# Optimization experiments

Hardware: AMD Instinct MI355X
Metric: run time of the kernel (lower is better)

Reference implementation:

```python
import jax, jax.numpy as jnp
import numpy as np

B, K, C, Q, NCLS = 16, 36, 2048, 1024, 16
LIN = 1024
DIN = 2 * C + 16 + Q  # 5136


def _linear_params(key, din, dout, scale=0.02):
    kw, kb = jax.random.split(key)
    W = jax.random.normal(kw, (din, dout), dtype=jnp.float32) * scale
    b = jax.random.normal(kb, (dout,), dtype=jnp.float32) * scale
    return W, b


def setup_inputs() -> dict:
    key = jax.random.key(0)
    ks = jax.random.split(key, 12)
    box_feats = jax.random.normal(ks[0], (B, K, C), dtype=jnp.float32)
    q_feats = jax.random.normal(ks[1], (B, Q), dtype=jnp.float32)
    # valid boxes: x2>x1, y2>y1 so areas are strictly positive (no div-by-zero)
    x1y1 = jax.random.uniform(ks[2], (B, K, 2), dtype=jnp.float32)
    wh = jax.random.uniform(ks[3], (B, K, 2), dtype=jnp.float32, minval=0.05, maxval=1.0)
    box_coords = jnp.concatenate([x1y1, x1y1 + wh, wh], axis=-1)  # [B,K,6]
    index = jax.random.randint(ks[4], (B,), 1, K + 1)  # ragged box counts in [1,K]
    wholefeat = jax.random.normal(ks[5], (B, C), dtype=jnp.float32)
    pooled = jax.random.normal(ks[6], (B, C), dtype=jnp.float32)
    W1, b1 = _linear_params(ks[7], DIN, LIN)
    W2, b2 = _linear_params(ks[8], LIN, LIN)
    W3, b3 = _linear_params(ks[9], LIN, LIN)
    Wf1, bf1 = _linear_params(ks[10], LIN, LIN // 2)
    Wf2, bf2 = _linear_params(ks[11], LIN // 2, NCLS)
    return {"wholefeat": wholefeat, "pooled": pooled, "box_feats": box_feats,
            "q_feats": q_feats, "box_coords": box_coords, "index": index,
            "W1": W1, "b1": b1, "W2": W2, "b2": b2, "W3": W3, "b3": b3,
            "Wf1": Wf1, "bf1": bf1, "Wf2": Wf2, "bf2": bf2}


def _rn_forward(box_feats, q_feats, box_coords, index,
                W1, b1, W2, b2, W3, b3, Wf1, bf1, Wf2, bf2):
    b_, k_, c_ = box_feats.shape
    # ragged -> padded + mask: pair (i,j) valid iff i < index[b] and j < index[b]
    valid = (jnp.arange(k_)[None, :] < index[:, None]).astype(box_feats.dtype)  # [B,K]
    pair_mask = valid[:, :, None] * valid[:, None, :]  # [B,K,K]

    # pairwise dot of region features
    dot = jnp.einsum('bid,bjd->bij', box_feats, box_feats)[..., None]  # [B,K,K,1]

    bc = box_coords  # [B,K,6]
    area = (bc[..., 2] - bc[..., 0]) * (bc[..., 3] - bc[..., 1])  # [B,K]
    lr = jnp.maximum(0.0, jnp.minimum(bc[:, :, None, 2], bc[:, None, :, 2])
                     - jnp.maximum(bc[:, :, None, 0], bc[:, None, :, 0]))
    ud = jnp.maximum(0.0, jnp.minimum(bc[:, :, None, 3], bc[:, None, :, 3])
                     - jnp.maximum(bc[:, :, None, 1], bc[:, None, :, 1]))
    overlap = lr * ud  # [B,K,K]
    area_i = area[:, :, None]
    area_j = area[:, None, :]
    iou = (overlap / (area_i + area_j - overlap))[..., None]
    o_ij = (overlap / area_i)[..., None]
    o_ji = (overlap / area_j)[..., None]

    b_ij = jnp.broadcast_to(bc[:, :, None, :], (b_, k_, k_, 6))
    b_ji = jnp.broadcast_to(bc[:, None, :, :], (b_, k_, k_, 6))
    o_i = jnp.broadcast_to(box_feats[:, :, None, :], (b_, k_, k_, c_))
    o_j = jnp.broadcast_to(box_feats[:, None, :, :], (b_, k_, k_, c_))
    qst = jnp.broadcast_to(q_feats[:, None, None, :], (b_, k_, k_, q_feats.shape[-1]))

    # [B,K,K,5136] = [o_i, o_j, qst, dot, b_ij, b_ji, iou, o_ij, o_ji]
    feat = jnp.concatenate([o_i, o_j, qst, dot, b_ij, b_ji, iou, o_ij, o_ji], axis=-1)

    h = jax.nn.relu(feat @ W1 + b1)
    h = jax.nn.relu(h @ W2 + b2)
    h = jax.nn.relu(h @ W3 + b3)  # [B,K,K,1024]

    # masked sum-pool over all valid (i,j) pairs
    g = jnp.einsum('bijh,bij->bh', h, pair_mask)  # [B,1024]

    out = jax.nn.relu(g @ Wf1 + bf1) @ Wf2 + bf2  # [B,Ncls]
    return out


def reference(wholefeat, pooled, box_feats, q_feats, box_coords, index,
              W1, b1, W2, b2, W3, b3, Wf1, bf1, Wf2, bf2):
    # wholefeat / pooled are unused by the original forward as well
    return _rn_forward(box_feats, q_feats, box_coords, index,
                       W1, b1, W2, b2, W3, b3, Wf1, bf1, Wf2, bf2)
```

## Files before the change

kernel.cpp:

```cpp
#include <hip/hip_runtime.h>
#include <stdint.h>

typedef unsigned short u16;
typedef __attribute__((ext_vector_type(8))) short short8;
typedef __attribute__((ext_vector_type(4))) float f32x4;

#define Bn 16
#define Kn 36
#define Cn 2048
#define Qn 1024
#define LINn 1024
#define NPp 1296
#define NPAIRn 20736
#define NBIn 576

__device__ __forceinline__ u16 f2bf(float f) {
  union { float f; unsigned int u; } v; v.f = f;
  unsigned int r = v.u + 0x7FFFu + ((v.u >> 16) & 1u);
  return (u16)(r >> 16);
}

__device__ __forceinline__ void llds16(const void* g, void* l) {
  __builtin_amdgcn_global_load_lds((const __attribute__((address_space(1))) void*)g,
                                   (__attribute__((address_space(3))) void*)l, 16, 0, 0);
}

__global__ void k_transpose_all(const float* __restrict__ W1, const float* __restrict__ W2,
                                const float* __restrict__ W3, u16* __restrict__ W1abT,
                                u16* __restrict__ W2T, u16* __restrict__ W3T) {
  __shared__ float tile[32][33];
  int z = blockIdx.z;
  const float* src; u16* dst; int ld_dst;
  if (z == 0)      { if (blockIdx.y >= 32) return; src = W2; dst = W2T; ld_dst = 1024; }
  else if (z == 1) { if (blockIdx.y >= 32) return; src = W3; dst = W3T; ld_dst = 1024; }
  else if (z == 2) { src = W1; dst = W1abT; ld_dst = 2048; }
  else             { src = W1 + (size_t)2048 * 1024; dst = W1abT + (size_t)1024 * 2048; ld_dst = 2048; }
  int n0 = blockIdx.x * 32, k0 = blockIdx.y * 32;
  int tx = threadIdx.x & 31, ty = threadIdx.x >> 5;
#pragma unroll
  for (int r = 0; r < 32; r += 8)
    tile[ty + r][tx] = src[(size_t)(k0 + ty + r) * 1024 + (n0 + tx)];
  __syncthreads();
#pragma unroll
  for (int r = 0; r < 32; r += 8)
    dst[(size_t)(n0 + ty + r) * ld_dst + (k0 + tx)] = f2bf(tile[tx][ty + r]);
}

__global__ void k_f2b(const float4* __restrict__ src, ushort4* __restrict__ dst, int n4) {
  int i = blockIdx.x * 256 + threadIdx.x;
  if (i < n4) {
    float4 v = src[i];
    ushort4 o;
    o.x = f2bf(v.x); o.y = f2bf(v.y); o.z = f2bf(v.z); o.w = f2bf(v.w);
    dst[i] = o;
  }
}

__global__ void k_build(const int* __restrict__ index, int* __restrict__ pairList,
                        int* __restrict__ batchC, int* __restrict__ cnt2) {
  __shared__ int offs[17];
  int tid = threadIdx.x;
  if (tid == 0) {
    int o = 0;
    for (int b = 0; b < Bn; ++b) { offs[b] = o; int v = index[b]; o += v * v; }
    offs[16] = o;
    cnt2[0] = o;
    cnt2[1] = (o + 127) & ~127;
  }
  __syncthreads();
  int total = offs[16];
  int totalPad = (total + 127) & ~127;
  for (int b = 0; b < Bn; ++b) {
    int v = index[b]; int n = v * v; int base = offs[b];
    for (int t = tid; t < n; t += 256) {
      int i = t / v, j = t - i * v;
      pairList[base + t] = b * NPp + i * Kn + j;
      batchC[base + t] = b;
    }
  }
  for (int t = total + tid; t < totalPad; t += 256) {
    pairList[t] = 0;
    batchC[t] = 0;
  }
}

__global__ void k_pcinit(const float* __restrict__ b1, float* __restrict__ Pc) {
  int n = blockIdx.x * 256 + threadIdx.x;
  float v = b1[n];
#pragma unroll
  for (int b = 0; b < Bn; ++b) Pc[b * LINn + n] = v;
}

__global__ void k_pconst(const float* __restrict__ q, const float* __restrict__ W1,
                         float* __restrict__ Pc) {
  __shared__ float qs[Bn][32];
  int n = blockIdx.x * 256 + threadIdx.x;
  int k0 = blockIdx.y * 32;
  const float* Wq = W1 + (size_t)(2 * Cn) * LINn;
  for (int t = threadIdx.x; t < Bn * 32; t += 256) {
    int b = t >> 5, k = t & 31;
    qs[b][k] = q[b * Qn + k0 + k];
  }
  __syncthreads();
  float acc[Bn];
#pragma unroll
  for (int b = 0; b < Bn; ++b) acc[b] = 0.f;
  for (int k = 0; k < 32; ++k) {
    float w = Wq[(size_t)(k0 + k) * LINn + n];
#pragma unroll
    for (int b = 0; b < Bn; ++b) acc[b] += qs[b][k] * w;
  }
#pragma unroll
  for (int b = 0; b < Bn; ++b) atomicAdd(&Pc[b * LINn + n], acc[b]);
}

__global__ void k_pairscalars(const float* __restrict__ bfm, const float* __restrict__ bc,
                              const int* __restrict__ pairList, const int* __restrict__ cnt2,
                              float* __restrict__ dotC, float* __restrict__ iouC,
                              float* __restrict__ oijC, float* __restrict__ ojiC) {
  int cnt = cnt2[0];
  int lane = threadIdx.x & 63;
  for (int m = blockIdx.x * 4 + (threadIdx.x >> 6); m < cnt; m += gridDim.x * 4) {
    int p = pairList[m];
    int b = p / NPp, rem = p - b * NPp, i = rem / Kn, j = rem - (rem / Kn) * Kn;
    const float4* Ai = (const float4*)(bfm + (size_t)(b * Kn + i) * Cn);
    const float4* Aj = (const float4*)(bfm + (size_t)(b * Kn + j) * Cn);
    float s = 0.f;
#pragma unroll
    for (int t = 0; t < Cn / 4 / 64; ++t) {
      float4 x = Ai[lane + t * 64], y = Aj[lane + t * 64];
      s += x.x * y.x + x.y * y.y + x.z * y.z + x.w * y.w;
    }
#pragma unroll
    for (int o = 32; o > 0; o >>= 1) s += __shfl_down(s, o);
    if (lane == 0) {
      const float* ci = bc + (size_t)(b * Kn + i) * 6;
      const float* cj = bc + (size_t)(b * Kn + j) * 6;
      float ai = (ci[2] - ci[0]) * (ci[3] - ci[1]);
      float aj = (cj[2] - cj[0]) * (cj[3] - cj[1]);
      float lr = fmaxf(0.f, fminf(ci[2], cj[2]) - fmaxf(ci[0], cj[0]));
      float ud = fmaxf(0.f, fminf(ci[3], cj[3]) - fmaxf(ci[1], cj[1]));
      float ov = lr * ud;
      dotC[m] = s;
      iouC[m] = ov / (ai + aj - ov);
      oijC[m] = ov / ai;
      ojiC[m] = ov / aj;
    }
  }
}

__global__ void k_padd(const float* __restrict__ P12s, const float* __restrict__ Pc,
                       const float* __restrict__ bc, const float* __restrict__ W1,
                       float* __restrict__ P12) {
  int bi = blockIdx.x;
  int b = bi / Kn;
  const float* c = bc + (size_t)bi * 6;
  const float* W = W1 + (size_t)(2 * Cn + Qn + 1) * LINn;
  const size_t SL = (size_t)640 * 2048;
#pragma unroll
  for (int it = 0; it < 8; ++it) {
    int cc = it * 256 + threadIdx.x;
    size_t idx = (size_t)bi * 2048 + cc;
    float s = P12s[idx] + P12s[SL + idx] + P12s[2 * SL + idx] + P12s[3 * SL + idx];
    int n = cc & 1023;
    int rbase = (cc < 1024) ? 0 : 6;
    float a = 0.f;
#pragma unroll
    for (int t = 0; t < 6; ++t) a += c[t] * W[(size_t)(rbase + t) * LINn + n];
    if (cc < 1024) a += Pc[b * LINn + n];
    P12[idx] = s + a;
  }
}

__global__ void k_h1(const float* __restrict__ P12,
                     const float* __restrict__ dotC, const float* __restrict__ iouC,
                     const float* __restrict__ oijC, const float* __restrict__ ojiC,
                     const int* __restrict__ pairList, const int* __restrict__ cnt2,
                     const float* __restrict__ W1, u16* __restrict__ H1) {
  int cnt = cnt2[0];
  int t = threadIdx.x;
  const float4* wd = (const float4*)(W1 + (size_t)(2 * Cn + Qn) * LINn);
  const float4* wu = (const float4*)(W1 + (size_t)(2 * Cn + Qn + 13) * LINn);
  const float4* wa = (const float4*)(W1 + (size_t)(2 * Cn + Qn + 14) * LINn);
  const float4* wb = (const float4*)(W1 + (size_t)(2 * Cn + Qn + 15) * LINn);
  float4 e1 = wd[t], e2 = wu[t], e3 = wa[t], e4 = wb[t];
  for (int m = blockIdx.x; m < cnt; m += gridDim.x) {
    int p = pairList[m];
    int b = p / NPp, rem = p - b * NPp, i = rem / Kn, j = rem - (rem / Kn) * Kn;
    float d = dotC[m], u = iouC[m], o1 = oijC[m], o2 = ojiC[m];
    const float4* p1 = (const float4*)(P12 + (size_t)(b * Kn + i) * 2048);
    const float4* p2 = (const float4*)(P12 + (size_t)(b * Kn + j) * 2048 + 1024);
    ushort4* outp = (ushort4*)(H1 + (size_t)m * 1024);
    float4 v1 = p1[t], v2 = p2[t];
    ushort4 o;
    o.x = f2bf(fmaxf(v1.x + v2.x + d * e1.x + u * e2.x + o1 * e3.x + o2 * e4.x, 0.f));
    o.y = f2bf(fmaxf(v1.y + v2.y + d * e1.y + u * e2.y + o1 * e3.y + o2 * e4.y, 0.f));
    o.z = f2bf(fmaxf(v1.z + v2.z + d * e1.z + u * e2.z + o1 * e3.z + o2 * e4.z, 0.f));
    o.w = f2bf(fmaxf(v1.w + v2.w + d * e1.w + u * e2.w + o1 * e3.w + o2 * e4.w, 0.f));
    outp[t] = o;
  }
}

template <int EPI>
__global__ void __launch_bounds__(256) k_gemm(
    const u16* __restrict__ A, const u16* __restrict__ BT,
    int N, int K, int KC, int Mvalid, const int* __restrict__ cnt2,
    float* __restrict__ Cf, int CfSlice, u16* __restrict__ Cb,
    const float* __restrict__ bias,
    const int* __restrict__ batchC, float* __restrict__ G) {
  __shared__ u16 Alds[2][128 * 64];
  __shared__ u16 Blds[2][64 * 64];
  __shared__ float Gpart[(EPI == 2) ? (Bn * 64) : 4];

  const int tid = threadIdx.x;
  const int wave = tid >> 6, lane = tid & 63;
  const int m0 = blockIdx.x * 128;
  const int n0 = blockIdx.y * 64;
  const int wm = (wave >> 1) * 64, wn = (wave & 1) * 32;

  int Mv = Mvalid;
  if (EPI != 0) {
    Mv = cnt2[0];
    if (m0 >= Mv) return;
  }
  if (EPI == 2) {
    for (int t = tid; t < Bn * 64; t += 256) Gpart[t] = 0.f;
  }

  f32x4 zero = {0.f, 0.f, 0.f, 0.f};
  f32x4 acc[4][2];
#pragma unroll
  for (int x = 0; x < 4; ++x)
#pragma unroll
    for (int y = 0; y < 2; ++y) acc[x][y] = zero;

  const int srow = tid >> 3;
  const int sslot = ((tid & 7) ^ (srow & 7)) * 16;
  const size_t ldb = (size_t)K * 2;

  auto stage = [&](int buf, int k0) {
    char* aB = (char*)Alds[buf] + wave * 1024;
    char* bB = (char*)Blds[buf] + wave * 1024;
#pragma unroll
    for (int c = 0; c < 4; ++c) {
      int rg = m0 + c * 32 + srow; if (rg >= Mv) rg = Mv - 1;
      llds16((const char*)A + (size_t)rg * ldb + (size_t)k0 * 2 + sslot, aB + c * 4096);
    }
#pragma unroll
    for (int c = 0; c < 2; ++c) {
      int rg = n0 + c * 32 + srow;
      llds16((const char*)BT + (size_t)rg * ldb + (size_t)k0 * 2 + sslot, bB + c * 4096);
    }
  };

  const int kbeg = blockIdx.z * KC;
  const int kend = kbeg + KC;
  stage(0, kbeg);
  asm volatile("s_waitcnt vmcnt(0)");
  __syncthreads();
  int cur = 0;
  for (int k0 = kbeg; k0 < kend; k0 += 64) {
    if (k0 + 64 < kend) stage(cur ^ 1, k0 + 64);
    const char* Ab = (const char*)Alds[cur];
    const char* Bb = (const char*)Blds[cur];
    short8 af[2][4], bfr[2][2];
#pragma unroll
    for (int kk = 0; kk < 2; ++kk) {
#pragma unroll
      for (int f = 0; f < 4; ++f) {
        int rA = wm + f * 16 + (lane & 15);
        int sl = ((kk * 4 + (lane >> 4)) ^ (rA & 7)) * 16;
        af[kk][f] = *(const short8*)(Ab + (size_t)rA * 128 + sl);
      }
#pragma unroll
      for (int f = 0; f < 2; ++f) {
        int rB = wn + f * 16 + (lane & 15);
        int sl = ((kk * 4 + (lane >> 4)) ^ (rB & 7)) * 16;
        bfr[kk][f] = *(const short8*)(Bb + (size_t)rB * 128 + sl);
      }
    }
#pragma unroll
    for (int kk = 0; kk < 2; ++kk)
#pragma unroll
      for (int x = 0; x < 4; ++x)
#pragma unroll
        for (int y = 0; y < 2; ++y)
          acc[x][y] = __builtin_amdgcn_mfma_f32_16x16x32_bf16(af[kk][x], bfr[kk][y],
                                                              acc[x][y], 0, 0, 0);
    asm volatile("s_waitcnt vmcnt(0)");
    __syncthreads();
    cur ^= 1;
  }

  if (EPI == 0) {
    float* Cs = Cf + (size_t)blockIdx.z * CfSlice;
#pragma unroll
    for (int x = 0; x < 4; ++x) {
      int rb = m0 + wm + x * 16 + (lane >> 4) * 4;
#pragma unroll
      for (int r = 0; r < 4; ++r) {
        int row = rb + r;
        if (row < Mv) {
#pragma unroll
          for (int y = 0; y < 2; ++y)
            Cs[(size_t)row * N + (n0 + wn + y * 16 + (lane & 15))] = acc[x][y][r];
        }
      }
    }
  } else if (EPI == 1) {
#pragma unroll
    for (int x = 0; x < 4; ++x) {
      int rb = m0 + wm + x * 16 + (lane >> 4) * 4;
#pragma unroll
      for (int r = 0; r < 4; ++r) {
        int row = rb + r;
#pragma unroll
        for (int y = 0; y < 2; ++y) {
          int col = n0 + wn + y * 16 + (lane & 15);
          Cb[(size_t)row * N + col] = f2bf(fmaxf(acc[x][y][r] + bias[col], 0.f));
        }
      }
    }
  } else {
    const int cnt = Mv;
#pragma unroll
    for (int x = 0; x < 4; ++x) {
      int rb = m0 + wm + x * 16 + (lane >> 4) * 4;
      int b0 = batchC[rb], b1 = batchC[rb + 1], b2 = batchC[rb + 2], b3 = batchC[rb + 3];
      float mk0 = (rb     < cnt) ? 1.f : 0.f;
      float mk1 = (rb + 1 < cnt) ? 1.f : 0.f;
      float mk2 = (rb + 2 < cnt) ? 1.f : 0.f;
      float mk3 = (rb + 3 < cnt) ? 1.f : 0.f;
#pragma unroll
      for (int y = 0; y < 2; ++y) {
        int coll = wn + y * 16 + (lane & 15);
        float bs = bias[n0 + coll];
        float s0 = mk0 * fmaxf(acc[x][y][0] + bs, 0.f);
        float s1 = mk1 * fmaxf(acc[x][y][1] + bs, 0.f);
        float s2 = mk2 * fmaxf(acc[x][y][2] + bs, 0.f);
        float s3 = mk3 * fmaxf(acc[x][y][3] + bs, 0.f);
        if (b0 == b3) {
          atomicAdd(&Gpart[b0 * 64 + coll], s0 + s1 + s2 + s3);
        } else {
          atomicAdd(&Gpart[b0 * 64 + coll], s0);
          atomicAdd(&Gpart[b1 * 64 + coll], s1);
          atomicAdd(&Gpart[b2 * 64 + coll], s2);
          atomicAdd(&Gpart[b3 * 64 + coll], s3);
        }
      }
    }
    __syncthreads();
    for (int t = tid; t < Bn * 64; t += 256) {
      float v = Gpart[t];
      if (v != 0.f) atomicAdd(&G[(t >> 6) * LINn + n0 + (t & 63)], v);
    }
  }
}

__global__ void k_final1(const float* __restrict__ G, const float* __restrict__ Wf1,
                         float* __restrict__ S) {
  __shared__ float g[128];
  int b = blockIdx.x, kz = blockIdx.y, tid = threadIdx.x;
  if (tid < 128) g[tid] = G[b * 1024 + kz * 128 + tid];
  __syncthreads();
  float acc = 0.f;
  const float* W = Wf1 + (size_t)(kz * 128) * 512 + tid;
  for (int k = 0; k < 128; ++k) acc += g[k] * W[(size_t)k * 512];
  atomicAdd(&S[b * 512 + tid], acc);
}

__global__ void k_final2(const float* __restrict__ S, const float* __restrict__ bf1,
                         const float* __restrict__ Wf2, const float* __restrict__ bf2,
                         float* __restrict__ out) {
  __shared__ float mid[512];
  __shared__ float part[256];
  int b = blockIdx.x, tid = threadIdx.x;
  for (int t = tid; t < 512; t += 256) mid[t] = fmaxf(S[b * 512 + t] + bf1[t], 0.f);
  __syncthreads();
  int o = tid & 15, seg = tid >> 4;
  float s = 0.f;
#pragma unroll
  for (int t = 0; t < 32; ++t) {
    int j = seg * 32 + t;
    s += mid[j] * Wf2[j * 16 + o];
  }
  part[tid] = s;
  __syncthreads();
  if (tid < 16) {
    float v = bf2[tid];
#pragma unroll
    for (int sg = 0; sg < 16; ++sg) v += part[sg * 16 + tid];
    out[b * 16 + tid] = v;
  }
}

extern "C" void kernel_launch(void* const* d_in, const int* in_sizes, int n_in,
                              void* d_out, int out_size, void* d_ws, size_t ws_size,
                              hipStream_t stream) {
  const float* box_feats  = (const float*)d_in[2];
  const float* q_feats    = (const float*)d_in[3];
  const float* box_coords = (const float*)d_in[4];
  const int*   index      = (const int*)d_in[5];
  const float* W1  = (const float*)d_in[6];
  const float* b1  = (const float*)d_in[7];
  const float* W2  = (const float*)d_in[8];
  const float* b2  = (const float*)d_in[9];
  const float* W3  = (const float*)d_in[10];
  const float* b3  = (const float*)d_in[11];
  const float* Wf1 = (const float*)d_in[12];
  const float* bf1 = (const float*)d_in[13];
  const float* Wf2 = (const float*)d_in[14];
  const float* bf2 = (const float*)d_in[15];
  float* out = (float*)d_out;

  char* ws = (char*)d_ws;
  size_t off = 0;
  auto alloc = [&](size_t bytes) { void* p = ws + off; off += (bytes + 255) & ~(size_t)255; return p; };
  u16* W1abT = (u16*)alloc((size_t)2048 * 2048 * 2);
  u16* W2T   = (u16*)alloc((size_t)1024 * 1024 * 2);
  u16* W3T   = (u16*)alloc((size_t)1024 * 1024 * 2);
  u16* BFb   = (u16*)alloc((size_t)NBIn * Cn * 2);
  float* P12s = (float*)alloc((size_t)4 * 640 * 2048 * 4);
  float* P12  = (float*)alloc((size_t)NBIn * 2048 * 4);
  float* Pc   = (float*)alloc((size_t)Bn * LINn * 4);
  float* dotC = (float*)alloc((size_t)NPAIRn * 4);
  float* iouC = (float*)alloc((size_t)NPAIRn * 4);
  float* oijC = (float*)alloc((size_t)NPAIRn * 4);
  float* ojiC = (float*)alloc((size_t)NPAIRn * 4);
  int* pairList = (int*)alloc((size_t)NPAIRn * 4);
  int* batchC   = (int*)alloc((size_t)NPAIRn * 4);
  int* cnt2     = (int*)alloc(64);
  float* G  = (float*)alloc((size_t)Bn * LINn * 4);
  float* S  = (float*)alloc((size_t)Bn * 512 * 4);
  u16* H1 = (u16*)alloc((size_t)NPAIRn * 1024 * 2);
  u16* H2 = (u16*)alloc((size_t)NPAIRn * 1024 * 2);

  k_transpose_all<<<dim3(32, 64, 4), 256, 0, stream>>>(W1, W2, W3, W1abT, W2T, W3T);
  k_f2b<<<(NBIn * Cn / 4 + 255) / 256, 256, 0, stream>>>((const float4*)box_feats,
                                                         (ushort4*)BFb, NBIn * Cn / 4);
  k_build<<<1, 256, 0, stream>>>(index, pairList, batchC, cnt2);
  k_pcinit<<<4, 256, 0, stream>>>(b1, Pc);
  k_pconst<<<dim3(4, 32), 256, 0, stream>>>(q_feats, W1, Pc);
  k_pairscalars<<<648, 256, 0, stream>>>(box_feats, box_coords, pairList, cnt2,
                                         dotC, iouC, oijC, ojiC);
  k_gemm<0><<<dim3(5, 32, 4), 256, 0, stream>>>(BFb, W1abT, 2048, 2048, 512, NBIn, nullptr,
                                                P12s, 640 * 2048, nullptr, nullptr,
                                                nullptr, nullptr);
  k_padd<<<NBIn, 256, 0, stream>>>(P12s, Pc, box_coords, W1, P12);
  k_h1<<<2592, 256, 0, stream>>>(P12, dotC, iouC, oijC, ojiC, pairList, cnt2, W1, H1);
  hipMemsetAsync(G, 0, (size_t)Bn * LINn * 4, stream);
  hipMemsetAsync(S, 0, (size_t)Bn * 512 * 4, stream);
  k_gemm<1><<<dim3(162, 16, 1), 256, 0, stream>>>(H1, W2T, 1024, 1024, 1024, 0, cnt2,
                                                  nullptr, 0, H2, b2, nullptr, nullptr);
  k_gemm<2><<<dim3(162, 16, 1), 256, 0, stream>>>(H2, W3T, 1024, 1024, 1024, 0, cnt2,
                                                  nullptr, 0, nullptr, b3, batchC, G);
  k_final1<<<dim3(16, 8), 512, 0, stream>>>(G, Wf1, S);
  k_final2<<<16, 256, 0, stream>>>(S, bf1, Wf2, bf2, out);
}
```

Measured before the change: 161.6 us.

## Triple-buffer GEMM LDS pipeline and remap blocks by XCD for active tiles

```diff
diff --git a/kernel.cpp b/kernel.cpp
--- a/kernel.cpp
+++ b/kernel.cpp
@@ -208,20 +208,30 @@
     float* __restrict__ Cf, int CfSlice, u16* __restrict__ Cb,
     const float* __restrict__ bias,
     const int* __restrict__ batchC, float* __restrict__ G) {
-  __shared__ u16 Alds[2][128 * 64];
-  __shared__ u16 Blds[2][64 * 64];
+  __shared__ u16 Alds[3][128 * 64];
+  __shared__ u16 Blds[3][64 * 64];
   __shared__ float Gpart[(EPI == 2) ? (Bn * 64) : 4];
 
   const int tid = threadIdx.x;
   const int wave = tid >> 6, lane = tid & 63;
-  const int m0 = blockIdx.x * 128;
-  const int n0 = blockIdx.y * 64;
   const int wm = (wave >> 1) * 64, wn = (wave & 1) * 32;
 
   int Mv = Mvalid;
-  if (EPI != 0) {
+  int m0, n0;
+  if (EPI == 0) {
+    m0 = blockIdx.x * 128;
+    n0 = blockIdx.y * 64;
+  } else {
     Mv = cnt2[0];
-    if (m0 >= Mv) return;
+    int nMt = (Mv + 127) >> 7;
+    int nact = nMt * 16;
+    int id = blockIdx.x;
+    if (id >= nact) return;
+    int q = nact >> 3, r = nact & 7;
+    int xcd = id & 7, rank = id >> 3;
+    int wg = (xcd < r ? xcd * (q + 1) : r * (q + 1) + (xcd - r) * q) + rank;
+    m0 = (wg >> 4) * 128;
+    n0 = (wg & 15) * 64;
   }
   if (EPI == 2) {
     for (int t = tid; t < Bn * 64; t += 256) Gpart[t] = 0.f;
@@ -253,16 +263,9 @@
     }
   };
 
-  const int kbeg = blockIdx.z * KC;
-  const int kend = kbeg + KC;
-  stage(0, kbeg);
-  asm volatile("s_waitcnt vmcnt(0)");
-  __syncthreads();
-  int cur = 0;
-  for (int k0 = kbeg; k0 < kend; k0 += 64) {
-    if (k0 + 64 < kend) stage(cur ^ 1, k0 + 64);
-    const char* Ab = (const char*)Alds[cur];
-    const char* Bb = (const char*)Blds[cur];
+  auto compute = [&](int buf) {
+    const char* Ab = (const char*)Alds[buf];
+    const char* Bb = (const char*)Blds[buf];
     short8 af[2][4], bfr[2][2];
 #pragma unroll
     for (int kk = 0; kk < 2; ++kk) {
@@ -287,10 +290,26 @@
         for (int y = 0; y < 2; ++y)
           acc[x][y] = __builtin_amdgcn_mfma_f32_16x16x32_bf16(af[kk][x], bfr[kk][y],
                                                               acc[x][y], 0, 0, 0);
-    asm volatile("s_waitcnt vmcnt(0)");
-    __syncthreads();
-    cur ^= 1;
-  }
+  };
+
+  const int kbeg = blockIdx.z * KC;
+  const int nt = KC >> 6;
+  stage(0, kbeg);
+  stage(1, kbeg + 64);
+  asm volatile("s_waitcnt vmcnt(6)" ::: "memory");
+  __builtin_amdgcn_s_barrier();
+  int t = 0;
+  for (; t + 2 < nt; ++t) {
+    stage((t + 2) % 3, kbeg + (t + 2) * 64);
+    compute(t % 3);
+    asm volatile("s_waitcnt vmcnt(6)" ::: "memory");
+    __builtin_amdgcn_s_barrier();
+  }
+  compute(t % 3);
+  asm volatile("s_waitcnt vmcnt(0)" ::: "memory");
+  __builtin_amdgcn_s_barrier();
+  ++t;
+  compute(t % 3);
 
   if (EPI == 0) {
     float* Cs = Cf + (size_t)blockIdx.z * CfSlice;
@@ -350,9 +369,9 @@
       }
     }
     __syncthreads();
-    for (int t = tid; t < Bn * 64; t += 256) {
-      float v = Gpart[t];
-      if (v != 0.f) atomicAdd(&G[(t >> 6) * LINn + n0 + (t & 63)], v);
+    for (int t2 = tid; t2 < Bn * 64; t2 += 256) {
+      float v = Gpart[t2];
+      if (v != 0.f) atomicAdd(&G[(t2 >> 6) * LINn + n0 + (t2 & 63)], v);
     }
   }
 }
@@ -450,9 +469,9 @@
   k_h1<<<2592, 256, 0, stream>>>(P12, dotC, iouC, oijC, ojiC, pairList, cnt2, W1, H1);
   hipMemsetAsync(G, 0, (size_t)Bn * LINn * 4, stream);
   hipMemsetAsync(S, 0, (size_t)Bn * 512 * 4, stream);
-  k_gemm<1><<<dim3(162, 16, 1), 256, 0, stream>>>(H1, W2T, 1024, 1024, 1024, 0, cnt2,
+  k_gemm<1><<<dim3(2592, 1, 1), 256, 0, stream>>>(H1, W2T, 1024, 1024, 1024, 0, cnt2,
                                                   nullptr, 0, H2, b2, nullptr, nullptr);
-  k_gemm<2><<<dim3(162, 16, 1), 256, 0, stream>>>(H2, W3T, 1024, 1024, 1024, 0, cnt2,
+  k_gemm<2><<<dim3(2592, 1, 1), 256, 0, stream>>>(H2, W3T, 1024, 1024, 1024, 0, cnt2,
                                                   nullptr, 0, nullptr, b3, batchC, G);
   k_final1<<<dim3(16, 8), 512, 0, stream>>>(G, Wf1, S);
   k_final2<<<16, 256, 0, stream>>>(S, bf1, Wf2, bf2, out);
```

Measured after the change: 202.7 us. +25.4%, slower.
